# Kernel optimization log

Hardware: AMD Instinct MI355X
Metric: run time of the kernel (lower is better)

The kernel has to match this reference:

```python
import jax, jax.numpy as jnp
import numpy as np

NB_NEIGHBORS = 8
NB_FEATURES = 2000


def setup_inputs() -> dict:
    key = jax.random.key(0)
    k1, k2 = jax.random.split(key)
    inputs = jax.random.normal(k1, (64, 2000, 16), dtype=jnp.float32)
    coordinates = jax.random.normal(k2, (512, 2000, 16), dtype=jnp.float32)
    return {"inputs": inputs, "coordinates": coordinates}


def reference(inputs, coordinates):
    # coordinates: (nb_coordinates, nb_features, filters)
    # inputs:      (batch, nb_features, filters)
    # Per-filter squared euclidean distances between feature columns.
    sq = jnp.sum(coordinates * coordinates, axis=0)            # (F, C)
    cross = jnp.einsum('cif,cjf->ijf', coordinates, coordinates)  # (F, F, C)
    dist = jnp.maximum(sq[None, :, :] + sq[:, None, :] - 2.0 * cross, 0.0)
    # top-k smallest distances along axis 1 (per feature, per filter)
    _, idx = jax.lax.top_k(jnp.transpose(-dist, (0, 2, 1)), NB_NEIGHBORS)  # (F, C, K)
    idx = jnp.transpose(idx, (0, 2, 1))[:NB_FEATURES, :NB_NEIGHBORS, :]    # (F, K, C)
    # Gather: out[b, i*K + j, c] = inputs[b, idx[i, j, c], c]
    B, _, C = inputs.shape
    idx_flat = idx.reshape(-1, C)                              # (F*K, C)
    gather_idx = jnp.broadcast_to(idx_flat[None], (B,) + idx_flat.shape)
    out = jnp.take_along_axis(inputs, gather_idx, axis=1)      # (B, F*K, C)
    return out
```

## Files before the change

### kernel.cpp

```cpp
#include <hip/hip_runtime.h>
#include <math.h>


#define F_TOT 2000
#define CF    16
#define KDIM  512
#define NB_K  8
#define IPAD  2048
#define NCAND 10
#define NCH   2
#define NCTOT (NCAND * NCH)

typedef __attribute__((ext_vector_type(8))) short bf16x8;
typedef __attribute__((ext_vector_type(4))) float f32x4;

__device__ inline unsigned short f2bf(float x) {
  unsigned int u = __float_as_uint(x);
  return (unsigned short)((u + 0x7fffu + ((u >> 16) & 1u)) >> 16);
}

#define GLOAD_LDS16(gp, lp)                                                          \
  __builtin_amdgcn_global_load_lds((const __attribute__((address_space(1))) void*)(gp), \
                                   (__attribute__((address_space(3))) void*)(lp), 16, 0, 0)

__global__ __launch_bounds__(256) void sq_kernel(const float* __restrict__ coords,
                                                 float* __restrict__ sq_out) {
  int i = blockIdx.x;
  int t = threadIdx.x;
  int f = t & 15;
  int cg = t >> 4;
  const float* base = coords + (size_t)i * CF + f;
  double s = 0.0;
  for (int c = cg * 32; c < cg * 32 + 32; ++c) {
    float v = base[(size_t)c * (F_TOT * CF)];
    s += (double)v * (double)v;
  }
  __shared__ double red[256];
  red[t] = s;
  __syncthreads();
  if (cg == 0) {
    double tot = 0.0;
#pragma unroll
    for (int g = 0; g < 16; ++g) tot += red[g * 16 + f];
    sq_out[i * CF + f] = (float)tot;
  }
}

__global__ __launch_bounds__(256) void cvt_bf16_kernel(const float* __restrict__ coords,
                                                       unsigned short* __restrict__ cbt) {
  __shared__ float lds[32 * 257];
  const int i0 = blockIdx.x * 16;
  const int c0 = blockIdx.y * 32;
  const int t = threadIdx.x;
  const int io = t >> 4, f = t & 15;
  const int iclamp = min(i0 + io, F_TOT - 1);
  for (int cc = 0; cc < 32; ++cc)
    lds[cc * 257 + t] = coords[(size_t)(c0 + cc) * (F_TOT * CF) + iclamp * CF + f];
  __syncthreads();
  size_t obase = ((size_t)f * IPAD + (i0 + io)) * KDIM + c0;
#pragma unroll
  for (int cc = 0; cc < 32; cc += 4) {
    unsigned int lo = (unsigned int)f2bf(lds[(cc + 0) * 257 + t]) |
                      ((unsigned int)f2bf(lds[(cc + 1) * 257 + t]) << 16);
    unsigned int hi = (unsigned int)f2bf(lds[(cc + 2) * 257 + t]) |
                      ((unsigned int)f2bf(lds[(cc + 3) * 257 + t]) << 16);
    *(uint2*)(cbt + obase + cc) = make_uint2(lo, hi);
  }
}

__global__ __launch_bounds__(256) void cvt_f32t_kernel(const float* __restrict__ coords,
                                                       float* __restrict__ ct) {
  __shared__ float lds[32 * 257];
  const int i0 = blockIdx.x * 16;
  const int c0 = blockIdx.y * 32;
  const int t = threadIdx.x;
  const int io = t >> 4;
  for (int cc = 0; cc < 32; ++cc)
    lds[cc * 257 + t] = coords[(size_t)(c0 + cc) * (F_TOT * CF) + i0 * CF + t];
  __syncthreads();
  const int f = t & 15;
  size_t obase = ((size_t)f * F_TOT + (i0 + io)) * KDIM + c0;
#pragma unroll
  for (int cc = 0; cc < 32; cc += 4) {
    float4 v = make_float4(lds[(cc + 0) * 257 + t], lds[(cc + 1) * 257 + t],
                           lds[(cc + 2) * 257 + t], lds[(cc + 3) * 257 + t]);
    *(float4*)(ct + obase + cc) = v;
  }
}

__global__ __launch_bounds__(256, 3) void approx_kernel(const unsigned short* __restrict__ cbt,
                                                        const float* __restrict__ sq,
                                                        int* __restrict__ cand) {
  const int bx = blockIdx.x;
  const int f = bx & 15;
  const int it = (bx >> 4) & 15;
  const int jc = bx >> 8;
  const int ibase = it * 128;
  const int jcbase = jc * 1000;
  const int jlimit = jcbase + 1000;

  const int t = threadIdx.x;
  const int lane = t & 63;
  const int w = t >> 6;
  const int wi = w & 1, wj = w >> 1;
  const int lrow = lane & 15, lq = lane >> 4;

  __shared__ char smem[50176];
  float* Dl = (float*)smem;
  float* sqj = (float*)(smem + 49152);

  const unsigned short* abase_g = cbt + ((size_t)f * IPAD + ibase) * KDIM;

  const int ii = t & 127;
  const int half = t >> 7;
  const bool rowok = (ibase + ii < F_TOT);

  float bv[NCAND]; int bi[NCAND];
#pragma unroll
  for (int k = 0; k < NCAND; ++k) { bv[k] = __builtin_inff(); bi[k] = 0x7fffffff; }
  float sqi = rowok ? sq[(ibase + ii) * CF + f] : 0.0f;

  int arow[4];
#pragma unroll
  for (int mi = 0; mi < 4; ++mi) arow[mi] = wi * 64 + mi * 16 + lrow;
  int brow[8];
#pragma unroll
  for (int nj = 0; nj < 8; ++nj) brow[nj] = wj * 128 + nj * 16 + lrow;

  for (int js = 0; js < 4; ++js) {
    const int jbase = jcbase + js * 256;
    __syncthreads();
    { int jg = jbase + t; sqj[t] = (jg < F_TOT) ? sq[jg * CF + f] : 0.0f; }

    f32x4 acc[4][8];
#pragma unroll
    for (int mi = 0; mi < 4; ++mi)
#pragma unroll
      for (int nj = 0; nj < 8; ++nj) acc[mi][nj] = (f32x4){0.f, 0.f, 0.f, 0.f};

    const unsigned short* bbase_g = cbt + ((size_t)f * IPAD + jbase) * KDIM;

#define STAGE32(q, c0)                                                                \
    {                                                                                 \
      char* Ad = smem + (q) * 24576;                                                  \
      char* Bd = Ad + 8192;                                                           \
      _Pragma("unroll")                                                               \
      for (int p = 0; p < 2; ++p) {                                                   \
        int s = p * 256 + t;                                                          \
        int r = s >> 2, sg = s & 3;                                                   \
        GLOAD_LDS16(abase_g + (size_t)r * KDIM + (c0) + ((sg ^ (r & 3)) << 3),        \
                    Ad + p * 4096 + (w << 10));                                       \
      }                                                                               \
      _Pragma("unroll")                                                               \
      for (int p = 0; p < 4; ++p) {                                                   \
        int s = p * 256 + t;                                                          \
        int r = s >> 2, sg = s & 3;                                                   \
        GLOAD_LDS16(bbase_g + (size_t)r * KDIM + (c0) + ((sg ^ (r & 3)) << 3),        \
                    Bd + p * 4096 + (w << 10));                                       \
      }                                                                               \
    }

    STAGE32(0, 0);

    for (int m = 0; m < 16; ++m) {
      const int cur = m & 1;
      const unsigned short* Al = (const unsigned short*)(smem + cur * 24576);
      const unsigned short* Bl = (const unsigned short*)(smem + cur * 24576 + 8192);
      __builtin_amdgcn_s_barrier();
      if (m < 15) {
        STAGE32((m + 1) & 1, (m + 1) * 32);
        asm volatile("s_waitcnt vmcnt(6)" ::: "memory");
      } else {
        asm volatile("s_waitcnt vmcnt(0)" ::: "memory");
      }
      __builtin_amdgcn_s_barrier();
      __builtin_amdgcn_sched_barrier(0);
      bf16x8 a[4];
#pragma unroll
      for (int mi = 0; mi < 4; ++mi)
        a[mi] = *(const bf16x8*)(Al + arow[mi] * 32 + ((lq ^ (arow[mi] & 3)) << 3));
#pragma unroll
      for (int nj = 0; nj < 8; ++nj) {
        bf16x8 b = *(const bf16x8*)(Bl + brow[nj] * 32 + ((lq ^ (brow[nj] & 3)) << 3));
#pragma unroll
        for (int mi = 0; mi < 4; ++mi)
          acc[mi][nj] = __builtin_amdgcn_mfma_f32_16x16x32_bf16(a[mi], b, acc[mi][nj], 0, 0, 0);
      }
    }
#undef STAGE32

#pragma unroll
    for (int ph = 0; ph < 4; ++ph) {
      __syncthreads();
      if (wj == (ph >> 1)) {
#pragma unroll
        for (int mi = 0; mi < 4; ++mi) {
#pragma unroll
          for (int njq = 0; njq < 4; ++njq) {
            int nj = (ph & 1) * 4 + njq;
#pragma unroll
            for (int r = 0; r < 4; ++r) {
              int row = wi * 64 + mi * 16 + lq * 4 + r;
              int col = njq * 16 + lrow;
              int q = col >> 2, rr = col & 3;
              Dl[row * 64 + (((q ^ (row & 7))) << 2) + rr] = acc[mi][nj][r];
            }
          }
        }
      }
      __syncthreads();
      if (rowok) {
        const int j0 = jbase + ph * 64 + half * 32;
        int cnt = jlimit - j0; if (cnt > 32) cnt = 32;
        for (int bb = 0; bb < 8; ++bb) {
          const int bo = bb * 4;
          if (bo >= cnt) break;
          const int qq = half * 8 + bb;
          const float4 g4 = *(const float4*)&Dl[ii * 64 + ((qq ^ (ii & 7)) << 2)];
          const float4 s4 = *(const float4*)&sqj[ph * 64 + half * 32 + bo];
          float d0 = fmaxf(fmaf(-2.0f, g4.x, sqi + s4.x), 0.0f);
          float d1 = fmaxf(fmaf(-2.0f, g4.y, sqi + s4.y), 0.0f);
          float d2 = fmaxf(fmaf(-2.0f, g4.z, sqi + s4.z), 0.0f);
          float d3 = fmaxf(fmaf(-2.0f, g4.w, sqi + s4.w), 0.0f);
          const int rem = cnt - bo;
          if (rem < 4) d3 = __builtin_inff();
          if (rem < 3) d2 = __builtin_inff();
          if (rem < 2) d1 = __builtin_inff();
          float mn = fminf(fminf(d0, d1), fminf(d2, d3));
          if (mn <= bv[NCAND - 1]) {
            float dd[4] = {d0, d1, d2, d3};
#pragma unroll
            for (int e = 0; e < 4; ++e) {
              float d = dd[e]; int jg = j0 + bo + e;
              if (d < bv[NCAND - 1] || (d == bv[NCAND - 1] && jg < bi[NCAND - 1])) {
                float cv = d; int ci = jg;
#pragma unroll
                for (int k = 0; k < NCAND; ++k) {
                  bool lt = (cv < bv[k]) || (cv == bv[k] && ci < bi[k]);
                  float tv = lt ? bv[k] : cv; int ti = lt ? bi[k] : ci;
                  bv[k] = lt ? cv : bv[k];    bi[k] = lt ? ci : bi[k];
                  cv = tv; ci = ti;
                }
              }
            }
          }
        }
      }
    }
  }

  __syncthreads();
  if (half == 1 && rowok) {
    float* wrow = &Dl[ii * 64];
#pragma unroll
    for (int k = 0; k < NCAND; ++k) { wrow[k] = bv[k]; *(int*)&wrow[NCAND + k] = bi[k]; }
  }
  __syncthreads();
  if (half == 0 && rowok) {
    const float* wrow = &Dl[ii * 64];
    float ov[NCAND]; int oi[NCAND];
#pragma unroll
    for (int k = 0; k < NCAND; ++k) { ov[k] = wrow[k]; oi[k] = *(const int*)&wrow[NCAND + k]; }
    float mv[NCAND]; int mj[NCAND];
    int p = 0, q = 0;
#pragma unroll
    for (int k = 0; k < NCAND; ++k) {
      bool mine = (q >= NCAND) || ((p < NCAND) &&
                  ((bv[p] < ov[q]) || (bv[p] == ov[q] && bi[p] < oi[q])));
      mv[k] = mine ? bv[p] : ov[q];
      mj[k] = mine ? bi[p] : oi[q];
      p += mine ? 1 : 0; q += mine ? 0 : 1;
    }
    (void)mv;
#pragma unroll
    for (int r = 0; r < NCAND; ++r) {
#pragma unroll
      for (int k = 0; k + 1 < NCAND; ++k) {
        if (((k ^ r) & 1) == 0) {
          int lo = min(mj[k], mj[k + 1]);
          int hi = max(mj[k], mj[k + 1]);
          mj[k] = lo; mj[k + 1] = hi;
        }
      }
    }
    int* dst = cand + ((size_t)(ibase + ii) * CF + f) * NCTOT + jc * NCAND;
#pragma unroll
    for (int k = 0; k < NCAND; ++k) dst[k] = mj[k];
  }
}

__global__ __launch_bounds__(256) void refine_dist_kernel(const float* __restrict__ ct,
                                                          const float* __restrict__ sq,
                                                          const int* __restrict__ cand,
                                                          float* __restrict__ dval) {
  const int NWG = (F_TOT * CF * (NCTOT / 2)) / 32;
  int orig = blockIdx.x;
  int bid = (orig & 7) * (NWG / 8) + (orig >> 3);
  int u = bid * 32 + (threadIdx.x >> 3);
  const int k = threadIdx.x & 7;
  int f = u / (F_TOT * (NCTOT / 2));
  int y = u - f * (F_TOT * (NCTOT / 2));
  int i = y / (NCTOT / 2);
  int m = y - i * (NCTOT / 2);
  int pf = i * CF + f;
  int j0 = cand[(size_t)pf * NCTOT + 2 * m];
  int j1 = cand[(size_t)pf * NCTOT + 2 * m + 1];
  const float* a = ct + ((size_t)f * F_TOT + i) * KDIM + k * 4;
  const float* p = ct + ((size_t)f * F_TOT + j0) * KDIM + k * 4;
  const float* q = ct + ((size_t)f * F_TOT + j1) * KDIM + k * 4;
  float g0 = 0.0f, g1 = 0.0f;
#pragma unroll
  for (int n = 0; n < 16; ++n) {
    float4 av = *(const float4*)(a + n * 32);
    float4 pv = *(const float4*)(p + n * 32);
    float4 qv = *(const float4*)(q + n * 32);
    g0 = fmaf(av.x, pv.x, g0); g1 = fmaf(av.x, qv.x, g1);
    g0 = fmaf(av.y, pv.y, g0); g1 = fmaf(av.y, qv.y, g1);
    g0 = fmaf(av.z, pv.z, g0); g1 = fmaf(av.z, qv.z, g1);
    g0 = fmaf(av.w, pv.w, g0); g1 = fmaf(av.w, qv.w, g1);
  }
#pragma unroll
  for (int off = 1; off < 8; off <<= 1) {
    g0 += __shfl_xor(g0, off);
    g1 += __shfl_xor(g1, off);
  }
  if (k == 0) {
    float sqi = sq[i * CF + f];
    float d0 = fmaf(-2.0f, g0, sqi + sq[j0 * CF + f]); d0 = fmaxf(d0, 0.0f);
    float d1 = fmaf(-2.0f, g1, sqi + sq[j1 * CF + f]); d1 = fmaxf(d1, 0.0f);
    dval[(size_t)pf * NCTOT + 2 * m]     = d0;
    dval[(size_t)pf * NCTOT + 2 * m + 1] = d1;
  }
}

__global__ __launch_bounds__(256) void select_kernel(const float* __restrict__ dval,
                                                     const int* __restrict__ cand,
                                                     int* __restrict__ fidx) {
  int pf = blockIdx.x * 256 + threadIdx.x;
  if (pf >= F_TOT * CF) return;
  int i = pf >> 4, f = pf & 15;
  float bval[NB_K]; int bidx[NB_K];
#pragma unroll
  for (int k = 0; k < NB_K; ++k) { bval[k] = __builtin_inff(); bidx[k] = 0; }
#pragma unroll
  for (int m = 0; m < NCTOT; ++m) {
    float d = dval[(size_t)pf * NCTOT + m];
    int j = cand[(size_t)pf * NCTOT + m];
    if (d < bval[NB_K - 1]) {
      float cv = d; int ci = j;
#pragma unroll
      for (int k = 0; k < NB_K; ++k)
        if (cv < bval[k]) {
          float tv = bval[k]; bval[k] = cv; cv = tv;
          int ti = bidx[k]; bidx[k] = ci; ci = ti;
        }
    }
  }
#pragma unroll
  for (int k = 0; k < NB_K; ++k)
    fidx[((size_t)i * NB_K + k) * CF + f] = bidx[k];
}

__global__ __launch_bounds__(256) void gather_kernel(const float* __restrict__ inputs,
                                                     const int* __restrict__ fidx,
                                                     float* __restrict__ out) {
  int b = blockIdx.y;
  int x = blockIdx.x * 256 + threadIdx.x;
  int c = x & 15;
  int n = fidx[x];
  out[(size_t)b * (F_TOT * NB_K * CF) + x] =
      inputs[(size_t)b * (F_TOT * CF) + n * CF + c];
}

extern "C" void kernel_launch(void* const* d_in, const int* in_sizes, int n_in,
                              void* d_out, int out_size, void* d_ws, size_t ws_size,
                              hipStream_t stream) {
  const float* inputs = (const float*)d_in[0];
  const float* coords = (const float*)d_in[1];
  float* out = (float*)d_out;

  unsigned short* cbt = (unsigned short*)d_out;
  float* ct = (float*)d_out;

  float* sq = (float*)d_ws;
  int* cand = (int*)d_ws + 32768;
  float* dval = (float*)d_ws + 32768 + 32000 * NCTOT;
  int* fidx = (int*)d_ws + 32768 + 2 * 32000 * NCTOT;

  sq_kernel<<<F_TOT, 256, 0, stream>>>(coords, sq);
  cvt_bf16_kernel<<<dim3(IPAD / 16, KDIM / 32), 256, 0, stream>>>(coords, cbt);
  approx_kernel<<<512, 256, 0, stream>>>(cbt, sq, cand);
  cvt_f32t_kernel<<<dim3(F_TOT / 16, KDIM / 32), 256, 0, stream>>>(coords, ct);
  refine_dist_kernel<<<(F_TOT * CF * (NCTOT / 2)) / 32, 256, 0, stream>>>(ct, sq, cand, dval);
  select_kernel<<<(F_TOT * CF + 255) / 256, 256, 0, stream>>>(dval, cand, fidx);
  dim3 g7((F_TOT * NB_K * CF) / 256, 64);
  gather_kernel<<<g7, 256, 0, stream>>>(inputs, fidx, out);
}
```

Before: 880.1 us.

## Split approx search into three j-chunks and fuse refine with select

The approximate bf16 candidate search now splits j into three chunks of 672 instead of two of 1000. This launches 768 workgroups at occupancy hint 2 and yields 30 candidates per point instead of 20. Exact refinement and top-8 selection are fused into one kernel: distances stay in LDS and the intermediate dval buffer and one launch are dropped. The cost is 50% more refinement work. Selection also runs on only two threads per 256-thread block, which may serialize badly.

Measured after the change: 802.4 us. -8.8%, faster.

```diff
diff --git a/kernel.cpp b/kernel.cpp
--- a/kernel.cpp
+++ b/kernel.cpp
@@ -6,9 +6,11 @@
 #define CF    16
 #define KDIM  512
 #define NB_K  8
-#define IPAD  2048
+#define IPAD  2112
 #define NCAND 10
-#define NCH   2
+#define NCH   3
+#define CHUNK 672
+#define JS_N  3
 #define NCTOT (NCAND * NCH)
 
 typedef __attribute__((ext_vector_type(8))) short bf16x8;
@@ -88,7 +90,7 @@
   }
 }
 
-__global__ __launch_bounds__(256, 3) void approx_kernel(const unsigned short* __restrict__ cbt,
+__global__ __launch_bounds__(256, 2) void approx_kernel(const unsigned short* __restrict__ cbt,
                                                         const float* __restrict__ sq,
                                                         int* __restrict__ cand) {
   const int bx = blockIdx.x;
@@ -96,8 +98,9 @@
   const int it = (bx >> 4) & 15;
   const int jc = bx >> 8;
   const int ibase = it * 128;
-  const int jcbase = jc * 1000;
-  const int jlimit = jcbase + 1000;
+  const int jcbase = jc * CHUNK;
+  int jlimit = jcbase + CHUNK;
+  if (jlimit > F_TOT) jlimit = F_TOT;
 
   const int t = threadIdx.x;
   const int lane = t & 63;
@@ -127,7 +130,7 @@
 #pragma unroll
   for (int nj = 0; nj < 8; ++nj) brow[nj] = wj * 128 + nj * 16 + lrow;
 
-  for (int js = 0; js < 4; ++js) {
+  for (int js = 0; js < JS_N; ++js) {
     const int jbase = jcbase + js * 256;
     __syncthreads();
     { int jg = jbase + t; sqj[t] = (jg < F_TOT) ? sq[jg * CF + f] : 0.0f; }
@@ -289,76 +292,81 @@
   }
 }
 
-__global__ __launch_bounds__(256) void refine_dist_kernel(const float* __restrict__ ct,
-                                                          const float* __restrict__ sq,
-                                                          const int* __restrict__ cand,
-                                                          float* __restrict__ dval) {
-  const int NWG = (F_TOT * CF * (NCTOT / 2)) / 32;
+__global__ __launch_bounds__(256) void refine_select_kernel(const float* __restrict__ ct,
+                                                            const float* __restrict__ sq,
+                                                            const int* __restrict__ cand,
+                                                            int* __restrict__ fidx) {
+  const int NWG = (F_TOT * CF) / 2;
   int orig = blockIdx.x;
   int bid = (orig & 7) * (NWG / 8) + (orig >> 3);
-  int u = bid * 32 + (threadIdx.x >> 3);
-  const int k = threadIdx.x & 7;
-  int f = u / (F_TOT * (NCTOT / 2));
-  int y = u - f * (F_TOT * (NCTOT / 2));
-  int i = y / (NCTOT / 2);
-  int m = y - i * (NCTOT / 2);
+  const int t = threadIdx.x;
+  const int u = t >> 3;
+  const int k = t & 7;
+  const int pl = u >> 4;
+  const int mu = u & 15;
+  __shared__ float lds_d[2 * NCTOT];
+
+  int P = bid * 2 + pl;
+  int f = P / F_TOT;
+  int i = P - f * F_TOT;
   int pf = i * CF + f;
-  int j0 = cand[(size_t)pf * NCTOT + 2 * m];
-  int j1 = cand[(size_t)pf * NCTOT + 2 * m + 1];
-  const float* a = ct + ((size_t)f * F_TOT + i) * KDIM + k * 4;
-  const float* p = ct + ((size_t)f * F_TOT + j0) * KDIM + k * 4;
-  const float* q = ct + ((size_t)f * F_TOT + j1) * KDIM + k * 4;
-  float g0 = 0.0f, g1 = 0.0f;
-#pragma unroll
-  for (int n = 0; n < 16; ++n) {
-    float4 av = *(const float4*)(a + n * 32);
-    float4 pv = *(const float4*)(p + n * 32);
-    float4 qv = *(const float4*)(q + n * 32);
-    g0 = fmaf(av.x, pv.x, g0); g1 = fmaf(av.x, qv.x, g1);
-    g0 = fmaf(av.y, pv.y, g0); g1 = fmaf(av.y, qv.y, g1);
-    g0 = fmaf(av.z, pv.z, g0); g1 = fmaf(av.z, qv.z, g1);
-    g0 = fmaf(av.w, pv.w, g0); g1 = fmaf(av.w, qv.w, g1);
-  }
-#pragma unroll
-  for (int off = 1; off < 8; off <<= 1) {
-    g0 += __shfl_xor(g0, off);
-    g1 += __shfl_xor(g1, off);
-  }
-  if (k == 0) {
-    float sqi = sq[i * CF + f];
-    float d0 = fmaf(-2.0f, g0, sqi + sq[j0 * CF + f]); d0 = fmaxf(d0, 0.0f);
-    float d1 = fmaf(-2.0f, g1, sqi + sq[j1 * CF + f]); d1 = fmaxf(d1, 0.0f);
-    dval[(size_t)pf * NCTOT + 2 * m]     = d0;
-    dval[(size_t)pf * NCTOT + 2 * m + 1] = d1;
-  }
-}
-
-__global__ __launch_bounds__(256) void select_kernel(const float* __restrict__ dval,
-                                                     const int* __restrict__ cand,
-                                                     int* __restrict__ fidx) {
-  int pf = blockIdx.x * 256 + threadIdx.x;
-  if (pf >= F_TOT * CF) return;
-  int i = pf >> 4, f = pf & 15;
-  float bval[NB_K]; int bidx[NB_K];
-#pragma unroll
-  for (int k = 0; k < NB_K; ++k) { bval[k] = __builtin_inff(); bidx[k] = 0; }
-#pragma unroll
-  for (int m = 0; m < NCTOT; ++m) {
-    float d = dval[(size_t)pf * NCTOT + m];
-    int j = cand[(size_t)pf * NCTOT + m];
-    if (d < bval[NB_K - 1]) {
-      float cv = d; int ci = j;
-#pragma unroll
-      for (int k = 0; k < NB_K; ++k)
-        if (cv < bval[k]) {
-          float tv = bval[k]; bval[k] = cv; cv = tv;
-          int ti = bidx[k]; bidx[k] = ci; ci = ti;
-        }
-    }
-  }
-#pragma unroll
-  for (int k = 0; k < NB_K; ++k)
-    fidx[((size_t)i * NB_K + k) * CF + f] = bidx[k];
+
+  if (mu < NCTOT / 2) {
+    int j0 = cand[(size_t)pf * NCTOT + 2 * mu];
+    int j1 = cand[(size_t)pf * NCTOT + 2 * mu + 1];
+    const float* a = ct + ((size_t)f * F_TOT + i) * KDIM + k * 4;
+    const float* p = ct + ((size_t)f * F_TOT + j0) * KDIM + k * 4;
+    const float* q = ct + ((size_t)f * F_TOT + j1) * KDIM + k * 4;
+    float g0 = 0.0f, g1 = 0.0f;
+#pragma unroll
+    for (int n = 0; n < 16; ++n) {
+      float4 av = *(const float4*)(a + n * 32);
+      float4 pv = *(const float4*)(p + n * 32);
+      float4 qv = *(const float4*)(q + n * 32);
+      g0 = fmaf(av.x, pv.x, g0); g1 = fmaf(av.x, qv.x, g1);
+      g0 = fmaf(av.y, pv.y, g0); g1 = fmaf(av.y, qv.y, g1);
+      g0 = fmaf(av.z, pv.z, g0); g1 = fmaf(av.z, qv.z, g1);
+      g0 = fmaf(av.w, pv.w, g0); g1 = fmaf(av.w, qv.w, g1);
+    }
+#pragma unroll
+    for (int off = 1; off < 8; off <<= 1) {
+      g0 += __shfl_xor(g0, off);
+      g1 += __shfl_xor(g1, off);
+    }
+    if (k == 0) {
+      float sqi = sq[i * CF + f];
+      float d0 = fmaf(-2.0f, g0, sqi + sq[j0 * CF + f]); d0 = fmaxf(d0, 0.0f);
+      float d1 = fmaf(-2.0f, g1, sqi + sq[j1 * CF + f]); d1 = fmaxf(d1, 0.0f);
+      lds_d[pl * NCTOT + 2 * mu]     = d0;
+      lds_d[pl * NCTOT + 2 * mu + 1] = d1;
+    }
+  }
+  __syncthreads();
+  if (t < 2) {
+    int P2 = bid * 2 + t;
+    int f2 = P2 / F_TOT;
+    int i2 = P2 - f2 * F_TOT;
+    int pf2 = i2 * CF + f2;
+    float bval[NB_K]; int bidx[NB_K];
+#pragma unroll
+    for (int kk = 0; kk < NB_K; ++kk) { bval[kk] = __builtin_inff(); bidx[kk] = 0; }
+    for (int mm = 0; mm < NCTOT; ++mm) {
+      float d = lds_d[t * NCTOT + mm];
+      int j = cand[(size_t)pf2 * NCTOT + mm];
+      if (d < bval[NB_K - 1]) {
+        float cv = d; int ci = j;
+#pragma unroll
+        for (int kk = 0; kk < NB_K; ++kk)
+          if (cv < bval[kk]) {
+            float tv = bval[kk]; bval[kk] = cv; cv = tv;
+            int ti = bidx[kk]; bidx[kk] = ci; ci = ti;
+          }
+      }
+    }
+#pragma unroll
+    for (int kk = 0; kk < NB_K; ++kk)
+      fidx[((size_t)i2 * NB_K + kk) * CF + f2] = bidx[kk];
+  }
 }
 
 __global__ __launch_bounds__(256) void gather_kernel(const float* __restrict__ inputs,
@@ -384,15 +392,13 @@
 
   float* sq = (float*)d_ws;
   int* cand = (int*)d_ws + 32768;
-  float* dval = (float*)d_ws + 32768 + 32000 * NCTOT;
-  int* fidx = (int*)d_ws + 32768 + 2 * 32000 * NCTOT;
+  int* fidx = (int*)d_ws + 32768 + 32000 * NCTOT;
 
   sq_kernel<<<F_TOT, 256, 0, stream>>>(coords, sq);
   cvt_bf16_kernel<<<dim3(IPAD / 16, KDIM / 32), 256, 0, stream>>>(coords, cbt);
-  approx_kernel<<<512, 256, 0, stream>>>(cbt, sq, cand);
+  approx_kernel<<<16 * 16 * NCH, 256, 0, stream>>>(cbt, sq, cand);
   cvt_f32t_kernel<<<dim3(F_TOT / 16, KDIM / 32), 256, 0, stream>>>(coords, ct);
-  refine_dist_kernel<<<(F_TOT * CF * (NCTOT / 2)) / 32, 256, 0, stream>>>(ct, sq, cand, dval);
-  select_kernel<<<(F_TOT * CF + 255) / 256, 256, 0, stream>>>(dval, cand, fidx);
+  refine_select_kernel<<<(F_TOT * CF) / 2, 256, 0, stream>>>(ct, sq, cand, fidx);
   dim3 g7((F_TOT * NB_K * CF) / 256, 64);
   gather_kernel<<<g7, 256, 0, stream>>>(inputs, fidx, out);
 }
```
